# Performance work log

Hardware: AMD Instinct MI355X
Metric: run time of the kernel (lower is better)

The kernel has to match this reference:

```python
import jax, jax.numpy as jnp
import numpy as np

B, S, D, H = 2, 2048, 1024, 16
DK = D // H  # 64
EPS = 1e-5


def setup_inputs() -> dict:
    key = jax.random.key(0)
    ks = jax.random.split(key, 12)
    sc = 1.0 / np.sqrt(D)
    inp = {
        "Q": jax.random.normal(ks[0], (B, S, D), jnp.float32),
        "K": jax.random.normal(ks[1], (B, S, D), jnp.float32),
        "V": jax.random.normal(ks[2], (B, S, D), jnp.float32),
        # causal mask: True = masked out
        "attn_mask": jnp.broadcast_to(jnp.triu(jnp.ones((S, S), bool), k=1), (B, S, S)),
        # torch Linear weights stored [out, in]
        "Wq": jax.random.normal(ks[3], (D, D), jnp.float32) * sc,
        "bq": jnp.zeros((D,), jnp.float32),
        "Wk": jax.random.normal(ks[4], (D, D), jnp.float32) * sc,
        "bk": jnp.zeros((D,), jnp.float32),
        "Wv": jax.random.normal(ks[5], (D, D), jnp.float32) * sc,
        "bv": jnp.zeros((D,), jnp.float32),
        "Wo": jax.random.normal(ks[6], (D, D), jnp.float32) * sc,
        "bo": jnp.zeros((D,), jnp.float32),
        "gamma": jnp.ones((D,), jnp.float32),
        "beta": jnp.zeros((D,), jnp.float32),
    }
    return inp


def _layer_norm(x, gamma, beta):
    mu = jnp.mean(x, axis=-1, keepdims=True)
    var = jnp.mean(jnp.square(x - mu), axis=-1, keepdims=True)
    return (x - mu) * jax.lax.rsqrt(var + EPS) * gamma + beta


def reference(Q, K, V, attn_mask, Wq, bq, Wk, bk, Wv, bv, Wo, bo, gamma, beta):
    residual = Q
    # projections -> [B, H, S, DK]
    q = (Q @ Wq.T + bq).reshape(B, S, H, DK).transpose(0, 2, 1, 3)
    k = (K @ Wk.T + bk).reshape(B, S, H, DK).transpose(0, 2, 1, 3)
    v = (V @ Wv.T + bv).reshape(B, S, H, DK).transpose(0, 2, 1, 3)
    scores = jnp.einsum("bhqd,bhkd->bhqk", q, k) / np.sqrt(DK)
    scores = jnp.where(attn_mask[:, None, :, :], -1e9, scores)
    attn = jax.nn.softmax(scores, axis=-1)
    ctx = jnp.einsum("bhqk,bhkd->bhqd", attn, v)  # [B,H,S,DK]
    ctx = ctx.transpose(0, 2, 1, 3).reshape(B, S, H * DK)
    out = ctx @ Wo.T + bo
    return _layer_norm(out + residual, gamma, beta), attn
```

## Files before the change

kernel.cpp:

```cpp
#include <hip/hip_runtime.h>
#include <hip/hip_fp16.h>

#define BB 2
#define SS 2048
#define DD 1024
#define HH 16
#define DKK 64
#define BHH (BB*HH)
#define MM (BB*SS)
#define EPSF 1e-5f

typedef _Float16 f16;
typedef _Float16 f16x4 __attribute__((ext_vector_type(4)));
typedef _Float16 f16x8 __attribute__((ext_vector_type(8)));
typedef float f32x4 __attribute__((ext_vector_type(4)));

__device__ __forceinline__ int swz128(int row, int byteInRow) {
    return row * 128 + (byteInRow ^ ((row & 7) << 4));
}

__device__ __forceinline__ void gl_lds16(const f16* g, f16* l) {
    __builtin_amdgcn_global_load_lds((const __attribute__((address_space(1))) void*)g,
                                     (__attribute__((address_space(3))) void*)l, 16, 0, 0);
}

__global__ __launch_bounds__(256) void cvt_pass(
    const float* __restrict__ s0, const float* __restrict__ s1, const float* __restrict__ s2,
    const float* __restrict__ s3, const float* __restrict__ s4, const float* __restrict__ s5,
    const float* __restrict__ s6,
    f16* __restrict__ d0, f16* __restrict__ d1, f16* __restrict__ d2,
    f16* __restrict__ d3, f16* __restrict__ d4, f16* __restrict__ d5, f16* __restrict__ d6)
{
    const int y = blockIdx.y;
    const float* s; f16* d; int n4;
    switch (y) {
        case 0: s = s0; d = d0; n4 = (MM * DD) / 4; break;
        case 1: s = s1; d = d1; n4 = (MM * DD) / 4; break;
        case 2: s = s2; d = d2; n4 = (MM * DD) / 4; break;
        case 3: s = s3; d = d3; n4 = (DD * DD) / 4; break;
        case 4: s = s4; d = d4; n4 = (DD * DD) / 4; break;
        case 5: s = s5; d = d5; n4 = (DD * DD) / 4; break;
        default: s = s6; d = d6; n4 = (DD * DD) / 4; break;
    }
    for (int i = blockIdx.x * 256 + threadIdx.x; i < n4; i += 256 * 256) {
        f32x4 v = ((const f32x4*)s)[i];
        f16x4 h = { (f16)v.x, (f16)v.y, (f16)v.z, (f16)v.w };
        ((f16x4*)d)[i] = h;
    }
}

__global__ __launch_bounds__(256) void qkv_gemm(
    const f16* __restrict__ Qf, const f16* __restrict__ Kf, const f16* __restrict__ Vf,
    const f16* __restrict__ Wqf, const float* __restrict__ bq,
    const f16* __restrict__ Wkf, const float* __restrict__ bk,
    const f16* __restrict__ Wvf, const float* __restrict__ bv,
    f16* __restrict__ qh, f16* __restrict__ kh, f16* __restrict__ vTh)
{
    const int type = blockIdx.z;
    const f16* X = (type == 0) ? Qf : (type == 1) ? Kf : Vf;
    const f16* W = (type == 0) ? Wqf : (type == 1) ? Wkf : Wvf;
    const float* bias = (type == 0) ? bq : (type == 1) ? bk : bv;
    const int m0 = blockIdx.y * 128, n0 = blockIdx.x * 128;

    __shared__ f16 smem[4][128 * 64];

    const int t = threadIdx.x;
    const int l = t & 63, w = t >> 6;
    const int c = l & 15, g = l >> 4;
    const int wr = (w >> 1) * 64, wc = (w & 1) * 64;

    f32x4 acc[4][4] = {};

    #define QKV_STAGE(kt, buf) { \
        _Pragma("unroll") \
        for (int p = 0; p < 4; p++) { \
            int idx = w * 4 + p; \
            int gci = idx * 64 + l; \
            int row = gci >> 3, slot = gci & 7; \
            int ss = slot ^ (row & 7); \
            gl_lds16(X + (size_t)(m0 + row) * DD + (kt) * 64 + ss * 8, smem[buf] + idx * 512); \
            gl_lds16(W + (size_t)(n0 + row) * DD + (kt) * 64 + ss * 8, smem[2 + (buf)] + idx * 512); \
        } }

    QKV_STAGE(0, 0);
    for (int k0 = 0; k0 < 16; k0++) {
        asm volatile("s_waitcnt vmcnt(0)");
        __builtin_amdgcn_s_barrier();
        __builtin_amdgcn_sched_barrier(0);
        if (k0 + 1 < 16) QKV_STAGE(k0 + 1, (k0 + 1) & 1);
        const f16* al = smem[k0 & 1];
        const f16* bl = smem[2 + (k0 & 1)];
        #pragma unroll
        for (int kk = 0; kk < 2; kk++) {
            f16x8 af[4], bf[4];
            #pragma unroll
            for (int mi = 0; mi < 4; mi++) {
                int row = wr + mi * 16 + c;
                af[mi] = *(const f16x8*)((const char*)al + swz128(row, kk * 64 + g * 16));
            }
            #pragma unroll
            for (int ni = 0; ni < 4; ni++) {
                int row = wc + ni * 16 + c;
                bf[ni] = *(const f16x8*)((const char*)bl + swz128(row, kk * 64 + g * 16));
            }
            __builtin_amdgcn_s_setprio(1);
            #pragma unroll
            for (int mi = 0; mi < 4; mi++)
                #pragma unroll
                for (int ni = 0; ni < 4; ni++)
                    acc[mi][ni] = __builtin_amdgcn_mfma_f32_16x16x32_f16(af[mi], bf[ni], acc[mi][ni], 0, 0, 0);
            __builtin_amdgcn_s_setprio(0);
        }
    }
    #undef QKV_STAGE

    const int b = m0 >> 11;
    const int mloc = m0 & (SS - 1);

    if (type == 2) {
        __syncthreads();
        f16* tb = smem[0];
        #pragma unroll
        for (int mi = 0; mi < 4; mi++) {
            #pragma unroll
            for (int ni = 0; ni < 4; ni++) {
                int nl = wc + ni * 16 + c;
                int mb = (wr + mi * 16 + g * 4) * 2;
                f16x4 hv;
                #pragma unroll
                for (int r = 0; r < 4; r++)
                    hv[r] = (f16)(acc[mi][ni][r] + bias[n0 + nl]);
                *(f16x4*)((char*)tb + nl * 256 + (mb ^ ((nl & 7) << 4))) = hv;
            }
        }
        __syncthreads();
        #pragma unroll
        for (int i = 0; i < 8; i++) {
            int o = w * 8192 + i * 1024 + l * 16;
            int nl = o >> 8;
            int inb = o & 255;
            f16x8 v = *(const f16x8*)((char*)tb + nl * 256 + (inb ^ ((nl & 7) << 4)));
            int ng = n0 + nl, h_ = ng >> 6, dk = ng & 63;
            int s = mloc + inb / 2;
            *(f16x8*)(vTh + ((size_t)((b * HH + h_) * DKK + dk)) * SS + s) = v;
        }
    } else {
        __syncthreads();
        f16* tb = smem[0];
        #pragma unroll
        for (int mi = 0; mi < 4; mi++) {
            #pragma unroll
            for (int ni = 0; ni < 4; ni++) {
                int nl = wc + ni * 16 + c;
                float bv_ = bias[n0 + nl];
                #pragma unroll
                for (int r = 0; r < 4; r++) {
                    int ml = wr + mi * 16 + g * 4 + r;
                    *(f16*)((char*)tb + ml * 256 + ((nl * 2) ^ ((ml & 7) << 4))) =
                        (f16)(acc[mi][ni][r] + bv_);
                }
            }
        }
        __syncthreads();
        f16* dst = (type == 0) ? qh : kh;
        #pragma unroll
        for (int i = 0; i < 8; i++) {
            int o = w * 8192 + i * 1024 + l * 16;
            int row = o >> 8, inb = o & 255;
            f16x8 v = *(const f16x8*)((char*)tb + row * 256 + (inb ^ ((row & 7) << 4)));
            int nl = inb / 2;
            int ng = n0 + nl, h_ = ng >> 6, dk = ng & 63;
            *(f16x8*)(dst + ((size_t)((b * HH + h_) * SS + mloc + row)) * DKK + dk) = v;
        }
    }
}

__global__ __launch_bounds__(256) void attn_kernel(
    const f16* __restrict__ qh, const f16* __restrict__ kh, const f16* __restrict__ vTh,
    float* __restrict__ attn_out, f16* __restrict__ ctx)
{
    const int bid = blockIdx.x;
    const int swz = (bid & 7) * 128 + (bid >> 3);
    const int bh = swz >> 5;
    const int qb = 31 - (swz & 31);
    const int qbase = qb * 64;
    const int t = threadIdx.x, l = t & 63, w = t >> 6;
    const int c = l & 15, g = l >> 4;

    __shared__ f16 kb3[3][64 * 64];
    __shared__ f16 vb3[3][64 * 64];

    const float CSC = 0.125f * 1.44269504f;
    const int nj = qb + 1;
    const int qloc = w * 16 + c;
    const int qglob = qbase + qloc;

    const f16* kbase = kh + (size_t)bh * SS * DKK;
    const f16* vbase = vTh + (size_t)bh * DKK * SS;
    float* aout = attn_out + (size_t)bh * SS * SS;

    const f16* qsrc = qh + (size_t)bh * SS * DKK + (size_t)qglob * DKK;
    f16x8 bq[2];
    bq[0] = *(const f16x8*)(qsrc + g * 8);
    bq[1] = *(const f16x8*)(qsrc + 32 + g * 8);

    #define STAGE_K(jt, buf) { \
        const f16* ksrc_ = kbase + (size_t)(jt) * 64 * DKK; \
        _Pragma("unroll") \
        for (int p = 0; p < 2; p++) { \
            int idx = w * 2 + p; \
            int gci = idx * 64 + l; \
            int row = gci >> 3, slot = gci & 7; \
            int ss_ = slot ^ (row & 7); \
            gl_lds16(ksrc_ + row * DKK + ss_ * 8, kb3[buf] + idx * 512); \
        } }
    #define STAGE_V(jt, buf) { \
        const f16* vsrc_ = vbase + (size_t)(jt) * 64; \
        _Pragma("unroll") \
        for (int p = 0; p < 2; p++) { \
            int idx = w * 2 + p; \
            int gci = idx * 64 + l; \
            int row = gci >> 3, slot = gci & 7; \
            int ss_ = slot ^ (row & 7); \
            gl_lds16(vsrc_ + (size_t)row * SS + ss_ * 8, vb3[buf] + idx * 512); \
        } }

    #define QKT(dstf, srcb) { \
        __builtin_amdgcn_s_setprio(1); \
        _Pragma("unroll") \
        for (int dw = 0; dw < 2; dw++) { \
            _Pragma("unroll") \
            for (int ni = 0; ni < 4; ni++) { \
                f16x8 ak = *(const f16x8*)((const char*)(srcb) + swz128(ni * 16 + c, dw * 64 + g * 16)); \
                dstf[ni] = __builtin_amdgcn_mfma_f32_16x16x32_f16(ak, bq[dw], dstf[ni], 0, 0, 0); \
            } \
        } \
        __builtin_amdgcn_s_setprio(0); }

    #define PSTORE(jt) { \
        float* pl_ = (float*)vb3; \
        _Pragma("unroll") \
        for (int i = 0; i < 4; i++) { \
            int row_ = w * 16 + 4 * i + g; \
            f32x4 v_ = *(const f32x4*)((char*)pl_ + row_ * 256 + ((c * 16) ^ ((row_ & 7) << 4))); \
            __builtin_nontemporal_store(v_, (f32x4*)(aout + (size_t)(qbase + row_) * SS + (jt) * 64 + c * 4)); \
        } }

    #define CBAR(n) { asm volatile("s_waitcnt vmcnt(" #n ")"); \
                      __builtin_amdgcn_s_barrier(); \
                      __builtin_amdgcn_sched_barrier(0); }

    STAGE_K(0, 0);
    if (nj > 1) STAGE_K(1, 1);
    STAGE_V(0, 0);
    CBAR(0);

    float lrow = 0.f;
    f32x4 cacc[4] = {};
    f32x4 sprev[4];

    for (int j = 0; j < nj; j++) {
        if (j + 2 < nj) STAGE_K(j + 2, (j + 2) % 3);
        if (j + 1 < nj) STAGE_V(j + 1, (j + 1) % 3);

        f32x4 scur[4] = {};
        QKT(scur, kb3[j % 3]);

        if (j > 0) {
            const f16* pvv = vb3[(j - 1) % 3];
            f16x4 bfr[4];
            #pragma unroll
            for (int ni = 0; ni < 4; ni++) {
                float e0 = exp2f(sprev[ni][0] * CSC);
                float e1 = exp2f(sprev[ni][1] * CSC);
                float e2 = exp2f(sprev[ni][2] * CSC);
                float e3 = exp2f(sprev[ni][3] * CSC);
                lrow += e0 + e1 + e2 + e3;
                bfr[ni] = f16x4{ (f16)e0, (f16)e1, (f16)e2, (f16)e3 };
            }
            __builtin_amdgcn_s_setprio(1);
            #pragma unroll
            for (int ni2 = 0; ni2 < 4; ni2++) {
                #pragma unroll
                for (int nk = 0; nk < 4; nk++) {
                    f16x4 av = *(const f16x4*)((const char*)pvv + swz128(ni2 * 16 + c, nk * 32 + g * 8));
                    cacc[ni2] = __builtin_amdgcn_mfma_f32_16x16x16f16(av, bfr[nk], cacc[ni2], 0, 0, 0);
                }
            }
            __builtin_amdgcn_s_setprio(0);
        }

        if (j + 3 <= nj)      CBAR(4)
        else if (j + 2 == nj) CBAR(2)
        else                  CBAR(0);

        #pragma unroll
        for (int x = 0; x < 4; x++) sprev[x] = scur[x];
    }

    STAGE_K(0, 0);
    if (nj > 1) STAGE_K(1, 1);

    {
        const f16* pvv = vb3[(nj - 1) % 3];
        f16x4 bfr[4];
        #pragma unroll
        for (int ni = 0; ni < 4; ni++) {
            int kkb = ni * 16 + 4 * g;
            float e0 = (kkb + 0 > qloc) ? 0.f : exp2f(sprev[ni][0] * CSC);
            float e1 = (kkb + 1 > qloc) ? 0.f : exp2f(sprev[ni][1] * CSC);
            float e2 = (kkb + 2 > qloc) ? 0.f : exp2f(sprev[ni][2] * CSC);
            float e3 = (kkb + 3 > qloc) ? 0.f : exp2f(sprev[ni][3] * CSC);
            lrow += e0 + e1 + e2 + e3;
            bfr[ni] = f16x4{ (f16)e0, (f16)e1, (f16)e2, (f16)e3 };
        }
        __builtin_amdgcn_s_setprio(1);
        #pragma unroll
        for (int ni2 = 0; ni2 < 4; ni2++) {
            #pragma unroll
            for (int nk = 0; nk < 4; nk++) {
                f16x4 av = *(const f16x4*)((const char*)pvv + swz128(ni2 * 16 + c, nk * 32 + g * 8));
                cacc[ni2] = __builtin_amdgcn_mfma_f32_16x16x16f16(av, bfr[nk], cacc[ni2], 0, 0, 0);
            }
        }
        __builtin_amdgcn_s_setprio(0);
    }

    lrow += __shfl_xor(lrow, 16);
    lrow += __shfl_xor(lrow, 32);
    const float rinv = 1.f / lrow;
    const float nls = -__log2f(lrow);

    {
        int b = bh >> 4, h_ = bh & 15;
        f16* cbase = ctx + (size_t)(b * SS + qglob) * DD + h_ * 64;
        #pragma unroll
        for (int ni2 = 0; ni2 < 4; ni2++) {
            f16x4 hv = { (f16)(cacc[ni2][0] * rinv), (f16)(cacc[ni2][1] * rinv),
                         (f16)(cacc[ni2][2] * rinv), (f16)(cacc[ni2][3] * rinv) };
            *(f16x4*)(cbase + ni2 * 16 + 4 * g) = hv;
        }
    }

    CBAR(0);

    {
        float* pl = (float*)vb3;
        for (int j = 0; j < nj; j++) {
            if (j + 2 < nj) STAGE_K(j + 2, (j + 2) % 3);

            f32x4 scur[4] = {};
            QKT(scur, kb3[j % 3]);

            if (j > 0) {
                #pragma unroll
                for (int ni = 0; ni < 4; ni++) {
                    f32x4 st = { exp2f(fmaf(sprev[ni][0], CSC, nls)),
                                 exp2f(fmaf(sprev[ni][1], CSC, nls)),
                                 exp2f(fmaf(sprev[ni][2], CSC, nls)),
                                 exp2f(fmaf(sprev[ni][3], CSC, nls)) };
                    *(f32x4*)((char*)pl + (w * 16 + c) * 256 + ((ni * 64 + g * 16) ^ ((c & 7) << 4))) = st;
                }
                PSTORE(j - 1);
            }

            if (j == 0 && j + 2 < nj)  CBAR(2)
            else if (j + 2 < nj)       CBAR(6)
            else if (j > 0)            CBAR(4)
            else                       CBAR(0);

            #pragma unroll
            for (int x = 0; x < 4; x++) sprev[x] = scur[x];
        }

        {
            #pragma unroll
            for (int ni = 0; ni < 4; ni++) {
                int kkb = ni * 16 + 4 * g;
                f32x4 st = { (kkb + 0 > qloc) ? 0.f : exp2f(fmaf(sprev[ni][0], CSC, nls)),
                             (kkb + 1 > qloc) ? 0.f : exp2f(fmaf(sprev[ni][1], CSC, nls)),
                             (kkb + 2 > qloc) ? 0.f : exp2f(fmaf(sprev[ni][2], CSC, nls)),
                             (kkb + 3 > qloc) ? 0.f : exp2f(fmaf(sprev[ni][3], CSC, nls)) };
                *(f32x4*)((char*)pl + (w * 16 + c) * 256 + ((ni * 64 + g * 16) ^ ((c & 7) << 4))) = st;
            }
            PSTORE(nj - 1);
        }
    }

    {
        f32x4 z = { 0.f, 0.f, 0.f, 0.f };
        for (int jb = qb + 1; jb < 32; jb++) {
            #pragma unroll
            for (int i = 0; i < 4; i++) {
                int c2 = t + 256 * i;
                int row = c2 >> 4, cg = c2 & 15;
                __builtin_nontemporal_store(z, (f32x4*)(aout + (size_t)(qbase + row) * SS + jb * 64 + cg * 4));
            }
        }
    }
    #undef STAGE_K
    #undef STAGE_V
    #undef QKT
    #undef PSTORE
    #undef CBAR
}

__global__ __launch_bounds__(256) void oproj_gemm(
    const f16* __restrict__ A, const f16* __restrict__ Wof, const float* __restrict__ bo,
    const float* __restrict__ resid, float* __restrict__ out)
{
    const int m0 = blockIdx.y * 128, n0 = blockIdx.x * 128;
    __shared__ f16 smem[4][128 * 64];
    const int t = threadIdx.x;
    const int l = t & 63, w = t >> 6;
    const int c = l & 15, g = l >> 4;
    const int wr = (w >> 1) * 64, wc = (w & 1) * 64;

    f32x4 acc[4][4] = {};

    #define OP_STAGE(kt, buf) { \
        _Pragma("unroll") \
        for (int p = 0; p < 4; p++) { \
            int idx = w * 4 + p; \
            int gci = idx * 64 + l; \
            int row = gci >> 3, slot = gci & 7; \
            int ss = slot ^ (row & 7); \
            gl_lds16(A + (size_t)(m0 + row) * DD + (kt) * 64 + ss * 8, smem[buf] + idx * 512); \
            gl_lds16(Wof + (size_t)(n0 + row) * DD + (kt) * 64 + ss * 8, smem[2 + (buf)] + idx * 512); \
        } }

    OP_STAGE(0, 0);
    for (int k0 = 0; k0 < 16; k0++) {
        asm volatile("s_waitcnt vmcnt(0)");
        __builtin_amdgcn_s_barrier();
        __builtin_amdgcn_sched_barrier(0);
        if (k0 + 1 < 16) OP_STAGE(k0 + 1, (k0 + 1) & 1);
        const f16* al = smem[k0 & 1];
        const f16* bl = smem[2 + (k0 & 1)];
        #pragma unroll
        for (int kk = 0; kk < 2; kk++) {
            f16x8 af[4], bf[4];
            #pragma unroll
            for (int mi = 0; mi < 4; mi++) {
                int row = wr + mi * 16 + c;
                af[mi] = *(const f16x8*)((const char*)al + swz128(row, kk * 64 + g * 16));
            }
            #pragma unroll
            for (int ni = 0; ni < 4; ni++) {
                int row = wc + ni * 16 + c;
                bf[ni] = *(const f16x8*)((const char*)bl + swz128(row, kk * 64 + g * 16));
            }
            __builtin_amdgcn_s_setprio(1);
            #pragma unroll
            for (int mi = 0; mi < 4; mi++)
                #pragma unroll
                for (int ni = 0; ni < 4; ni++)
                    acc[mi][ni] = __builtin_amdgcn_mfma_f32_16x16x32_f16(af[mi], bf[ni], acc[mi][ni], 0, 0, 0);
            __builtin_amdgcn_s_setprio(0);
        }
    }
    #undef OP_STAGE

    __syncthreads();
    float* tb = (float*)smem;
    #pragma unroll
    for (int mi = 0; mi < 4; mi++) {
        #pragma unroll
        for (int ni = 0; ni < 4; ni++) {
            int nl = wc + ni * 16 + c;
            #pragma unroll
            for (int r = 0; r < 4; r++) {
                int ml = wr + mi * 16 + g * 4 + r;
                *(float*)((char*)tb + ml * 512 + ((nl * 4) ^ ((ml & 7) << 4))) = acc[mi][ni][r];
            }
        }
    }
    __syncthreads();
    #pragma unroll
    for (int i = 0; i < 16; i++) {
        int o = w * 16384 + i * 1024 + l * 16;
        int row = o >> 9, inb = o & 511;
        f32x4 v = *(const f32x4*)((char*)tb + row * 512 + (inb ^ ((row & 7) << 4)));
        int nl = inb / 4;
        int n = n0 + nl, m = m0 + row;
        f32x4 bo4 = *(const f32x4*)(bo + n);
        f32x4 rs4 = *(const f32x4*)(resid + (size_t)m * DD + n);
        v = v + bo4 + rs4;
        *(f32x4*)(out + (size_t)m * DD + n) = v;
    }
}

__global__ __launch_bounds__(256) void ln_kernel(
    const float* __restrict__ x, const float* __restrict__ gamma,
    const float* __restrict__ beta, float* __restrict__ out)
{
    int row = blockIdx.x;
    int t = threadIdx.x;
    float4 v = ((const float4*)(x + (size_t)row * DD))[t];
    float s = v.x + v.y + v.z + v.w;
    __shared__ float red[4];
    #pragma unroll
    for (int o = 32; o; o >>= 1) s += __shfl_down(s, o, 64);
    if ((t & 63) == 0) red[t >> 6] = s;
    __syncthreads();
    float mean = (red[0] + red[1] + red[2] + red[3]) * (1.f / DD);
    __syncthreads();
    float4 d;
    d.x = v.x - mean; d.y = v.y - mean; d.z = v.z - mean; d.w = v.w - mean;
    float q = d.x * d.x + d.y * d.y + d.z * d.z + d.w * d.w;
    #pragma unroll
    for (int o = 32; o; o >>= 1) q += __shfl_down(q, o, 64);
    if ((t & 63) == 0) red[t >> 6] = q;
    __syncthreads();
    float var = (red[0] + red[1] + red[2] + red[3]) * (1.f / DD);
    float rstd = rsqrtf(var + EPSF);
    float4 g = ((const float4*)gamma)[t];
    float4 bt = ((const float4*)beta)[t];
    float4 o4;
    o4.x = d.x * rstd * g.x + bt.x;
    o4.y = d.y * rstd * g.y + bt.y;
    o4.z = d.z * rstd * g.z + bt.z;
    o4.w = d.w * rstd * g.w + bt.w;
    ((float4*)(out + (size_t)row * DD))[t] = o4;
}

extern "C" void kernel_launch(void* const* d_in, const int* in_sizes, int n_in,
                              void* d_out, int out_size, void* d_ws, size_t ws_size,
                              hipStream_t stream)
{
    const float* Q     = (const float*)d_in[0];
    const float* K     = (const float*)d_in[1];
    const float* V     = (const float*)d_in[2];
    const float* Wq    = (const float*)d_in[4];
    const float* bq    = (const float*)d_in[5];
    const float* Wk    = (const float*)d_in[6];
    const float* bk    = (const float*)d_in[7];
    const float* Wv    = (const float*)d_in[8];
    const float* bv    = (const float*)d_in[9];
    const float* Wo    = (const float*)d_in[10];
    const float* bo    = (const float*)d_in[11];
    const float* gamma = (const float*)d_in[12];
    const float* beta  = (const float*)d_in[13];

    float* out_ln   = (float*)d_out;
    float* attn_out = (float*)d_out + (size_t)BB * SS * DD;

    f16* Qf  = (f16*)attn_out;
    f16* Kf  = Qf + (size_t)MM * DD;
    f16* Vf  = Kf + (size_t)MM * DD;
    f16* Wqf = (f16*)out_ln;
    f16* Wkf = Wqf + (size_t)DD * DD;
    f16* Wvf = Wkf + (size_t)DD * DD;
    f16* Wof = Wvf + (size_t)DD * DD;

    char* ws = (char*)d_ws;
    f16*   qh    = (f16*)(ws);
    f16*   kh    = (f16*)(ws + ((size_t)8  << 20));
    f16*   vTh   = (f16*)(ws + ((size_t)16 << 20));
    f16*   ctx   = (f16*)(ws + ((size_t)24 << 20));
    float* oproj = (float*)(ws + ((size_t)32 << 20));

    cvt_pass<<<dim3(256, 7), 256, 0, stream>>>(Q, K, V, Wq, Wk, Wv, Wo,
                                               Qf, Kf, Vf, Wqf, Wkf, Wvf, Wof);
    qkv_gemm<<<dim3(8, 32, 3), 256, 0, stream>>>(Qf, Kf, Vf, Wqf, bq, Wkf, bk, Wvf, bv, qh, kh, vTh);
    attn_kernel<<<dim3(1024), 256, 0, stream>>>(qh, kh, vTh, attn_out, ctx);
    oproj_gemm<<<dim3(8, 32), 256, 0, stream>>>(ctx, Wof, bo, Q, oproj);
    ln_kernel<<<dim3(MM), 256, 0, stream>>>(oproj, gamma, beta, out_ln);
}
```

Before: 207.7 us.

## Rebalance cast pass, interleave causal query blocks, store pre-LN output as fp16

The conversion kernel now launches 512x4 blocks, and the four weight matrices are merged into one grid row so the work is spread more evenly. The attention kernel reorders query blocks so heavy and light causal tiles alternate, which balances per-block work across CUs. The output projection writes its pre-LayerNorm sum as fp16 instead of fp32, and the LN kernel reads fp16. This halves that intermediate traffic but rounds the residual sum to fp16 before normalization, which costs accuracy.

```diff
diff --git a/kernel.cpp b/kernel.cpp
--- a/kernel.cpp
+++ b/kernel.cpp
@@ -32,20 +32,26 @@
     f16* __restrict__ d3, f16* __restrict__ d4, f16* __restrict__ d5, f16* __restrict__ d6)
 {
     const int y = blockIdx.y;
-    const float* s; f16* d; int n4;
-    switch (y) {
-        case 0: s = s0; d = d0; n4 = (MM * DD) / 4; break;
-        case 1: s = s1; d = d1; n4 = (MM * DD) / 4; break;
-        case 2: s = s2; d = d2; n4 = (MM * DD) / 4; break;
-        case 3: s = s3; d = d3; n4 = (DD * DD) / 4; break;
-        case 4: s = s4; d = d4; n4 = (DD * DD) / 4; break;
-        case 5: s = s5; d = d5; n4 = (DD * DD) / 4; break;
-        default: s = s6; d = d6; n4 = (DD * DD) / 4; break;
-    }
-    for (int i = blockIdx.x * 256 + threadIdx.x; i < n4; i += 256 * 256) {
-        f32x4 v = ((const f32x4*)s)[i];
-        f16x4 h = { (f16)v.x, (f16)v.y, (f16)v.z, (f16)v.w };
-        ((f16x4*)d)[i] = h;
+    if (y < 3) {
+        const float* s = (y == 0) ? s0 : (y == 1) ? s1 : s2;
+        f16* d = (y == 0) ? d0 : (y == 1) ? d1 : d2;
+        const int n4 = (MM * DD) / 4;
+        for (int i = blockIdx.x * 256 + threadIdx.x; i < n4; i += 512 * 256) {
+            f32x4 v = ((const f32x4*)s)[i];
+            f16x4 h = { (f16)v.x, (f16)v.y, (f16)v.z, (f16)v.w };
+            ((f16x4*)d)[i] = h;
+        }
+    } else {
+        const int n4 = (DD * DD) / 4;
+        for (int i = blockIdx.x * 256 + threadIdx.x; i < 4 * n4; i += 512 * 256) {
+            int tsel = i >> 18;
+            int off = i & (n4 - 1);
+            const float* s = (tsel == 0) ? s3 : (tsel == 1) ? s4 : (tsel == 2) ? s5 : s6;
+            f16* d = (tsel == 0) ? d3 : (tsel == 1) ? d4 : (tsel == 2) ? d5 : d6;
+            f32x4 v = ((const f32x4*)s)[off];
+            f16x4 h = { (f16)v.x, (f16)v.y, (f16)v.z, (f16)v.w };
+            ((f16x4*)d)[off] = h;
+        }
     }
 }
 
@@ -182,7 +188,8 @@
     const int bid = blockIdx.x;
     const int swz = (bid & 7) * 128 + (bid >> 3);
     const int bh = swz >> 5;
-    const int qb = 31 - (swz & 31);
+    const int qs = swz & 31;
+    const int qb = (qs & 1) ? (qs >> 1) : 31 - (qs >> 1);
     const int qbase = qb * 64;
     const int t = threadIdx.x, l = t & 63, w = t >> 6;
     const int c = l & 15, g = l >> 4;
@@ -407,7 +414,7 @@
 
 __global__ __launch_bounds__(256) void oproj_gemm(
     const f16* __restrict__ A, const f16* __restrict__ Wof, const float* __restrict__ bo,
-    const float* __restrict__ resid, float* __restrict__ out)
+    const float* __restrict__ resid, f16* __restrict__ out)
 {
     const int m0 = blockIdx.y * 128, n0 = blockIdx.x * 128;
     __shared__ f16 smem[4][128 * 64];
@@ -486,17 +493,19 @@
         f32x4 bo4 = *(const f32x4*)(bo + n);
         f32x4 rs4 = *(const f32x4*)(resid + (size_t)m * DD + n);
         v = v + bo4 + rs4;
-        *(f32x4*)(out + (size_t)m * DD + n) = v;
+        f16x4 hv = { (f16)v.x, (f16)v.y, (f16)v.z, (f16)v.w };
+        *(f16x4*)(out + (size_t)m * DD + n) = hv;
     }
 }
 
 __global__ __launch_bounds__(256) void ln_kernel(
-    const float* __restrict__ x, const float* __restrict__ gamma,
+    const f16* __restrict__ x, const float* __restrict__ gamma,
     const float* __restrict__ beta, float* __restrict__ out)
 {
     int row = blockIdx.x;
     int t = threadIdx.x;
-    float4 v = ((const float4*)(x + (size_t)row * DD))[t];
+    f16x4 xv = ((const f16x4*)(x + (size_t)row * DD))[t];
+    float4 v = { (float)xv[0], (float)xv[1], (float)xv[2], (float)xv[3] };
     float s = v.x + v.y + v.z + v.w;
     __shared__ float red[4];
     #pragma unroll
@@ -558,9 +567,9 @@
     f16*   kh    = (f16*)(ws + ((size_t)8  << 20));
     f16*   vTh   = (f16*)(ws + ((size_t)16 << 20));
     f16*   ctx   = (f16*)(ws + ((size_t)24 << 20));
-    float* oproj = (float*)(ws + ((size_t)32 << 20));
-
-    cvt_pass<<<dim3(256, 7), 256, 0, stream>>>(Q, K, V, Wq, Wk, Wv, Wo,
+    f16*   oproj = (f16*)(ws + ((size_t)32 << 20));
+
+    cvt_pass<<<dim3(512, 4), 256, 0, stream>>>(Q, K, V, Wq, Wk, Wv, Wo,
                                                Qf, Kf, Vf, Wqf, Wkf, Wvf, Wof);
     qkv_gemm<<<dim3(8, 32, 3), 256, 0, stream>>>(Qf, Kf, Vf, Wqf, bq, Wkf, bk, Wvf, bv, qh, kh, vTh);
     attn_kernel<<<dim3(1024), 256, 0, stream>>>(qh, kh, vTh, attn_out, ctx);
```

New measurement: 222.8 us. +7.3%, slower.
